# Kernel optimization log

Measured on AMD Instinct MI355X. Metric: run time of the kernel, lower is better.

Reference implementation:

```python
import jax, jax.numpy as jnp
import numpy as np

B, CDD, HIS, T, L, D, K = 64, 5, 100, 30, 3, 256, 10
THRESHOLD = 0.1


def setup_inputs() -> dict:
    key = jax.random.key(0)
    k1, k2, k3, k4 = jax.random.split(key, 4)
    cdd_repr = jax.random.normal(k1, (B, CDD, D), dtype=jnp.float32)
    his_repr = jax.random.normal(k2, (B, HIS, D), dtype=jnp.float32)
    his_embedding = jax.random.normal(k3, (B, HIS, T, L, D), dtype=jnp.float32)
    # xavier_normal init for Linear(D, D)
    W_sel = jax.random.normal(k4, (D, D), dtype=jnp.float32) * np.sqrt(2.0 / (D + D))
    b_sel = jnp.zeros((D,), dtype=jnp.float32)
    return {"cdd_repr": cdd_repr, "his_repr": his_repr,
            "his_embedding": his_embedding, "W_sel": W_sel, "b_sel": b_sel}


def _l2_normalize(x, eps=1e-12):
    # matches torch F.normalize(dim=-1)
    n = jnp.linalg.norm(x, axis=-1, keepdims=True)
    return x / jnp.maximum(n, eps)


def reference(cdd_repr, his_repr, his_embedding, W_sel, b_sel):
    # selectionProject (Linear) + L2 normalize
    cdd_p = _l2_normalize(cdd_repr @ W_sel.T + b_sel)   # [B, CDD, D]
    his_p = _l2_normalize(his_repr @ W_sel.T + b_sel)   # [B, HIS, D]

    # news-level attention scores [B, CDD, HIS]
    attn = jnp.einsum('bcd,bhd->bch', cdd_p, his_p)

    # top-k over history
    attn_topk, idx = jax.lax.top_k(attn, K)             # [B, CDD, K]

    # multi-dim gather of history embeddings -> [B, CDD, K, T, L, D]
    his_activated = his_embedding[jnp.arange(B)[:, None, None], idx]

    # threshold masking: zero out weights below threshold, scale embeddings
    w = jnp.where(attn_topk < THRESHOLD, 0.0, attn_topk)
    his_activated = his_activated * w[:, :, :, None, None, None]

    return his_activated, idx
```

## Files before the change

### kernel.cpp

```cpp
#include <hip/hip_runtime.h>
#include <hip/hip_bf16.h>

#define NB   64
#define NCDD 5
#define NHIS 100
#define ND   256
#define NK   10
#define TLD  23040
#define THRESH 0.1f
#define NEG_INF (-3.402823466e38f)
#define NROWS_HIS 6400
#define NROWS_CDD 320

typedef float f32x4 __attribute__((ext_vector_type(4)));

__global__ __launch_bounds__(256) void proj_norm_all(
    const float* __restrict__ his_repr,
    const float* __restrict__ cdd_repr,
    const float* __restrict__ W,
    const float* __restrict__ bvec,
    float* __restrict__ Yall)
{
    __shared__ float red[4][8];
    const int r0  = blockIdx.x * 8;
    const int tid = threadIdx.x;
    const int sub = tid & 3;
    const int grp = tid >> 2;
    const int wave = tid >> 6, lane = tid & 63;

    const float* __restrict__ X = (r0 < NROWS_HIS)
        ? (his_repr + (size_t)r0 * ND)
        : (cdd_repr + (size_t)(r0 - NROWS_HIS) * ND);

    float acc[4][8];
#pragma unroll
    for (int p = 0; p < 4; ++p)
#pragma unroll
        for (int r = 0; r < 8; ++r) acc[p][r] = 0.f;

#pragma unroll 4
    for (int i = 0; i < 16; ++i) {
        const int kb = sub * 4 + 16 * i;
        float4 x4[8];
#pragma unroll
        for (int r = 0; r < 8; ++r)
            x4[r] = *(const float4*)(X + (size_t)r * ND + kb);
#pragma unroll
        for (int p = 0; p < 4; ++p) {
            const int d = p * 64 + grp;
            const float4 w4 = *(const float4*)(W + (size_t)d * ND + kb);
#pragma unroll
            for (int r = 0; r < 8; ++r)
                acc[p][r] += w4.x * x4[r].x + w4.y * x4[r].y
                           + w4.z * x4[r].z + w4.w * x4[r].w;
        }
    }

#pragma unroll
    for (int p = 0; p < 4; ++p)
#pragma unroll
        for (int r = 0; r < 8; ++r) {
            float v = acc[p][r];
            v += __shfl_xor(v, 1);
            v += __shfl_xor(v, 2);
            acc[p][r] = v;
        }

    float bias[4];
#pragma unroll
    for (int p = 0; p < 4; ++p) bias[p] = bvec[p * 64 + grp];

    float ss[8];
#pragma unroll
    for (int r = 0; r < 8; ++r) {
        float t = 0.f;
#pragma unroll
        for (int p = 0; p < 4; ++p) {
            const float y = acc[p][r] + bias[p];
            acc[p][r] = y;
            t += y * y;
        }
        for (int off = 32; off; off >>= 1) t += __shfl_xor(t, off);
        ss[r] = t;
    }
    if (lane == 0) {
#pragma unroll
        for (int r = 0; r < 8; ++r) red[wave][r] = ss[r];
    }
    __syncthreads();

#pragma unroll
    for (int r = 0; r < 8; ++r) {
        const float s = 0.25f * (red[0][r] + red[1][r] + red[2][r] + red[3][r]);
        const float scale = 1.0f / fmaxf(sqrtf(s), 1e-12f);
        if (sub == 0) {
#pragma unroll
            for (int p = 0; p < 4; ++p)
                Yall[(size_t)(r0 + r) * ND + p * 64 + grp] = acc[p][r] * scale;
        }
    }
}

__global__ __launch_bounds__(512) void attn_topk_kernel(
    const float* __restrict__ cdd_p,
    const float* __restrict__ his_p,
    float* __restrict__ out_idx_f,
    int* __restrict__ ws_idx,
    float* __restrict__ ws_w)
{
    __shared__ float attn_s[NCDD][128];
    const int b   = blockIdx.x;
    const int tid = threadIdx.x;
    const int sub = tid & 3, grp = tid >> 2;
    const int wave = tid >> 6, lane = tid & 63;

    const float* __restrict__ cbase = cdd_p + (size_t)b * NCDD * ND;
    const float* __restrict__ hbase = his_p + (size_t)b * NHIS * ND;

#pragma unroll
    for (int it = 0; it < 4; ++it) {
        const int task = it * 128 + grp;
        if (task < NCDD * NHIS) {
            const int c = task / NHIS, h = task - c * NHIS;
            const float* __restrict__ crow = cbase + (size_t)c * ND;
            const float* __restrict__ hrow = hbase + (size_t)h * ND;
            float a = 0.f;
#pragma unroll
            for (int i = 0; i < 16; ++i) {
                const int kb = sub * 4 + 16 * i;
                const float4 cv = *(const float4*)(crow + kb);
                const float4 hv = *(const float4*)(hrow + kb);
                a += cv.x * hv.x + cv.y * hv.y + cv.z * hv.z + cv.w * hv.w;
            }
            a += __shfl_xor(a, 1);
            a += __shfl_xor(a, 2);
            if (sub == 0) attn_s[c][h] = a;
        }
    }
    __syncthreads();

    if (wave < NCDD) {
        const int c = wave;
        float v0 = attn_s[c][lane];
        float v1 = (lane + 64 < NHIS) ? attn_s[c][lane + 64] : NEG_INF;
#pragma unroll
        for (int k = 0; k < NK; ++k) {
            float lv; int li;
            if (v1 > v0) { lv = v1; li = lane + 64; }
            else         { lv = v0; li = lane; }
            for (int off = 1; off < 64; off <<= 1) {
                const float ov = __shfl_xor(lv, off);
                const int   oi = __shfl_xor(li, off);
                if (ov > lv || (ov == lv && oi < li)) { lv = ov; li = oi; }
            }
            if (lane == 0) {
                const float w = (lv < THRESH) ? 0.0f : lv;
                const int g = (b * NCDD + c) * NK + k;
                ws_idx[g] = li;
                ws_w[g]   = w;
                out_idx_f[g] = (float)li;
            }
            if (li == lane)            v0 = NEG_INF;
            else if (li == lane + 64)  v1 = NEG_INF;
        }
    }
}

__global__ __launch_bounds__(256) void gather_kernel(
    const float* __restrict__ his_emb,
    const int* __restrict__ ws_idx,
    const float* __restrict__ ws_w,
    float* __restrict__ out)
{
    const int orig = blockIdx.x;
    const int g = (orig & 7) * 400 + (orig >> 3);
    const int b = g / (NCDD * NK);
    const int tid = threadIdx.x;
    const float w = ws_w[g];

    f32x4* __restrict__ dst = (f32x4*)(out + (size_t)g * TLD);

    if (w == 0.0f) {
        const f32x4 z = {0.f, 0.f, 0.f, 0.f};
#pragma unroll
        for (int it = 0; it < 22; ++it) dst[tid + it * 256] = z;
        if (tid < 128) dst[22 * 256 + tid] = z;
        return;
    }

    const int idx = ws_idx[g];
    const f32x4* __restrict__ src =
        (const f32x4*)(his_emb + ((size_t)b * NHIS + idx) * TLD);

    f32x4 v[22];
    f32x4 vt;
#pragma unroll
    for (int j = 0; j < 22; ++j) v[j] = src[tid + j * 256];
    const bool tail = (tid < 128);
    if (tail) vt = src[22 * 256 + tid];

#pragma unroll
    for (int j = 0; j < 22; ++j) dst[tid + j * 256] = v[j] * w;
    if (tail) dst[22 * 256 + tid] = vt * w;
}

extern "C" void kernel_launch(void* const* d_in, const int* in_sizes, int n_in,
                              void* d_out, int out_size, void* d_ws, size_t ws_size,
                              hipStream_t stream)
{
    const float* cdd_repr = (const float*)d_in[0];
    const float* his_repr = (const float*)d_in[1];
    const float* his_emb  = (const float*)d_in[2];
    const float* W_sel    = (const float*)d_in[3];
    const float* b_sel    = (const float*)d_in[4];
    float* out = (float*)d_out;

    char* ws = (char*)d_ws;
    float* Yall  = (float*)ws;
    float* his_p = Yall;
    float* cdd_p = Yall + (size_t)NROWS_HIS * ND;
    int*   idx_i = (int*)  (ws + 6881280);
    float* w_w   = (float*)(ws + 6894080);

    float* out_idx_f = out + (size_t)NB * NCDD * NK * TLD;

    proj_norm_all<<<(NROWS_HIS + NROWS_CDD) / 8, 256, 0, stream>>>(
        his_repr, cdd_repr, W_sel, b_sel, Yall);
    attn_topk_kernel<<<NB, 512, 0, stream>>>(cdd_p, his_p,
                                             out_idx_f, idx_i, w_w);
    gather_kernel<<<NB * NCDD * NK, 256, 0, stream>>>(his_emb, idx_i, w_w, out);
}
```

Before: 162.3 us.

## Fuse attention top-k into gather kernel, recomputing scores per output block

Merges the attention/top-k kernel into the gather kernel, so each gather block recomputes the 100 attention scores for its (b,c) row and the top-10 selection, then picks its own k-th entry. This removes one kernel launch and the workspace round-trip for indices and weights. In exchange the attention dot products and top-k are computed redundantly 10 times per (b,c), and the gather start is delayed by that compute in every block.

```diff
diff --git a/kernel.cpp b/kernel.cpp
--- a/kernel.cpp
+++ b/kernel.cpp
@@ -101,50 +101,58 @@
     }
 }
 
-__global__ __launch_bounds__(512) void attn_topk_kernel(
+__global__ __launch_bounds__(256) void attn_gather_kernel(
     const float* __restrict__ cdd_p,
     const float* __restrict__ his_p,
+    const float* __restrict__ his_emb,
     float* __restrict__ out_idx_f,
-    int* __restrict__ ws_idx,
-    float* __restrict__ ws_w)
+    float* __restrict__ out)
 {
-    __shared__ float attn_s[NCDD][128];
-    const int b   = blockIdx.x;
+    __shared__ float attn_s[128];
+    __shared__ float pick_w[NK];
+    __shared__ int   pick_i[NK];
+
+    const int orig = blockIdx.x;
+    const int g = (orig & 7) * 400 + (orig >> 3);
+    const int b = g / (NCDD * NK);
+    const int c = (g / NK) % NCDD;
+    const int k = g % NK;
     const int tid = threadIdx.x;
     const int sub = tid & 3, grp = tid >> 2;
     const int wave = tid >> 6, lane = tid & 63;
 
-    const float* __restrict__ cbase = cdd_p + (size_t)b * NCDD * ND;
+    const float* __restrict__ crow = cdd_p + ((size_t)b * NCDD + c) * ND;
     const float* __restrict__ hbase = his_p + (size_t)b * NHIS * ND;
-
-#pragma unroll
-    for (int it = 0; it < 4; ++it) {
-        const int task = it * 128 + grp;
-        if (task < NCDD * NHIS) {
-            const int c = task / NHIS, h = task - c * NHIS;
-            const float* __restrict__ crow = cbase + (size_t)c * ND;
-            const float* __restrict__ hrow = hbase + (size_t)h * ND;
-            float a = 0.f;
-#pragma unroll
-            for (int i = 0; i < 16; ++i) {
-                const int kb = sub * 4 + 16 * i;
-                const float4 cv = *(const float4*)(crow + kb);
-                const float4 hv = *(const float4*)(hrow + kb);
-                a += cv.x * hv.x + cv.y * hv.y + cv.z * hv.z + cv.w * hv.w;
+    {
+        const int h0 = grp, h1 = grp + 64;
+        const float* __restrict__ h0row = hbase + (size_t)h0 * ND;
+        const float* __restrict__ h1row = hbase + (size_t)h1 * ND;
+        float a0 = 0.f, a1 = 0.f;
+#pragma unroll
+        for (int i = 0; i < 16; ++i) {
+            const int kb = sub * 4 + 16 * i;
+            const float4 cv = *(const float4*)(crow + kb);
+            const float4 v0 = *(const float4*)(h0row + kb);
+            a0 += cv.x * v0.x + cv.y * v0.y + cv.z * v0.z + cv.w * v0.w;
+            if (h1 < NHIS) {
+                const float4 v1 = *(const float4*)(h1row + kb);
+                a1 += cv.x * v1.x + cv.y * v1.y + cv.z * v1.z + cv.w * v1.w;
             }
-            a += __shfl_xor(a, 1);
-            a += __shfl_xor(a, 2);
-            if (sub == 0) attn_s[c][h] = a;
+        }
+        a0 += __shfl_xor(a0, 1); a0 += __shfl_xor(a0, 2);
+        a1 += __shfl_xor(a1, 1); a1 += __shfl_xor(a1, 2);
+        if (sub == 0) {
+            attn_s[h0] = a0;
+            if (h1 < NHIS) attn_s[h1] = a1;
         }
     }
     __syncthreads();
 
-    if (wave < NCDD) {
-        const int c = wave;
-        float v0 = attn_s[c][lane];
-        float v1 = (lane + 64 < NHIS) ? attn_s[c][lane + 64] : NEG_INF;
-#pragma unroll
-        for (int k = 0; k < NK; ++k) {
+    if (wave == 0) {
+        float v0 = attn_s[lane];
+        float v1 = (lane + 64 < NHIS) ? attn_s[lane + 64] : NEG_INF;
+#pragma unroll
+        for (int kk = 0; kk < NK; ++kk) {
             float lv; int li;
             if (v1 > v0) { lv = v1; li = lane + 64; }
             else         { lv = v0; li = lane; }
@@ -154,29 +162,18 @@
                 if (ov > lv || (ov == lv && oi < li)) { lv = ov; li = oi; }
             }
             if (lane == 0) {
-                const float w = (lv < THRESH) ? 0.0f : lv;
-                const int g = (b * NCDD + c) * NK + k;
-                ws_idx[g] = li;
-                ws_w[g]   = w;
-                out_idx_f[g] = (float)li;
+                pick_i[kk] = li;
+                pick_w[kk] = (lv < THRESH) ? 0.0f : lv;
             }
             if (li == lane)            v0 = NEG_INF;
             else if (li == lane + 64)  v1 = NEG_INF;
         }
     }
-}
-
-__global__ __launch_bounds__(256) void gather_kernel(
-    const float* __restrict__ his_emb,
-    const int* __restrict__ ws_idx,
-    const float* __restrict__ ws_w,
-    float* __restrict__ out)
-{
-    const int orig = blockIdx.x;
-    const int g = (orig & 7) * 400 + (orig >> 3);
-    const int b = g / (NCDD * NK);
-    const int tid = threadIdx.x;
-    const float w = ws_w[g];
+    __syncthreads();
+
+    const int   idx = pick_i[k];
+    const float w   = pick_w[k];
+    if (tid == 0) out_idx_f[g] = (float)idx;
 
     f32x4* __restrict__ dst = (f32x4*)(out + (size_t)g * TLD);
 
@@ -188,7 +185,6 @@
         return;
     }
 
-    const int idx = ws_idx[g];
     const f32x4* __restrict__ src =
         (const f32x4*)(his_emb + ((size_t)b * NHIS + idx) * TLD);
 
@@ -219,14 +215,11 @@
     float* Yall  = (float*)ws;
     float* his_p = Yall;
     float* cdd_p = Yall + (size_t)NROWS_HIS * ND;
-    int*   idx_i = (int*)  (ws + 6881280);
-    float* w_w   = (float*)(ws + 6894080);
 
     float* out_idx_f = out + (size_t)NB * NCDD * NK * TLD;
 
     proj_norm_all<<<(NROWS_HIS + NROWS_CDD) / 8, 256, 0, stream>>>(
         his_repr, cdd_repr, W_sel, b_sel, Yall);
-    attn_topk_kernel<<<NB, 512, 0, stream>>>(cdd_p, his_p,
-                                             out_idx_f, idx_i, w_w);
-    gather_kernel<<<NB * NCDD * NK, 256, 0, stream>>>(his_emb, idx_i, w_w, out);
+    attn_gather_kernel<<<NB * NCDD * NK, 256, 0, stream>>>(
+        cdd_p, his_p, his_emb, out_idx_f, out);
 }
```

Measured after the change: 178.3 us. +9.9%, slower.

## Replace per-slot gather blocks with flat grid-stride gather over output

Applied to the files above, without the earlier changes.

The gather stage no longer launches one 256-thread block per (batch, candidate, k) slot with 23 float4s held per thread. It now uses a fixed grid of 2048 blocks that stride over the whole output as flat float4 elements, computing the slot index by integer division and reading the weight and index for each element. The aim is to even out load across the GPU and hide memory latency through a persistent grid-stride pattern. In exchange, every element pays a division plus repeated (cached) loads of the weight and index, and the explicit block-to-slot interleaving used for channel spreading is lost.

```diff
diff --git a/kernel.cpp b/kernel.cpp
--- a/kernel.cpp
+++ b/kernel.cpp
@@ -7,10 +7,12 @@
 #define ND   256
 #define NK   10
 #define TLD  23040
+#define NSLOT4 (3200 * 5760)
 #define THRESH 0.1f
 #define NEG_INF (-3.402823466e38f)
 #define NROWS_HIS 6400
 #define NROWS_CDD 320
+#define GBLOCKS 2048
 
 typedef float f32x4 __attribute__((ext_vector_type(4)));
 
@@ -166,42 +168,29 @@
     }
 }
 
-__global__ __launch_bounds__(256) void gather_kernel(
+__global__ __launch_bounds__(256) void gather_flat(
     const float* __restrict__ his_emb,
     const int* __restrict__ ws_idx,
     const float* __restrict__ ws_w,
     float* __restrict__ out)
 {
-    const int orig = blockIdx.x;
-    const int g = (orig & 7) * 400 + (orig >> 3);
-    const int b = g / (NCDD * NK);
-    const int tid = threadIdx.x;
-    const float w = ws_w[g];
-
-    f32x4* __restrict__ dst = (f32x4*)(out + (size_t)g * TLD);
-
-    if (w == 0.0f) {
-        const f32x4 z = {0.f, 0.f, 0.f, 0.f};
-#pragma unroll
-        for (int it = 0; it < 22; ++it) dst[tid + it * 256] = z;
-        if (tid < 128) dst[22 * 256 + tid] = z;
-        return;
-    }
-
-    const int idx = ws_idx[g];
-    const f32x4* __restrict__ src =
-        (const f32x4*)(his_emb + ((size_t)b * NHIS + idx) * TLD);
-
-    f32x4 v[22];
-    f32x4 vt;
-#pragma unroll
-    for (int j = 0; j < 22; ++j) v[j] = src[tid + j * 256];
-    const bool tail = (tid < 128);
-    if (tail) vt = src[22 * 256 + tid];
-
-#pragma unroll
-    for (int j = 0; j < 22; ++j) dst[tid + j * 256] = v[j] * w;
-    if (tail) dst[22 * 256 + tid] = vt * w;
+    const int S = GBLOCKS * 256;
+    const f32x4* __restrict__ src4 = (const f32x4*)his_emb;
+    f32x4* __restrict__ dst4 = (f32x4*)out;
+
+#pragma unroll 4
+    for (int i = blockIdx.x * 256 + threadIdx.x; i < NSLOT4; i += S) {
+        const int g = i / 5760;
+        const int r = i - g * 5760;
+        const float w = ws_w[g];
+        f32x4 v = {0.f, 0.f, 0.f, 0.f};
+        if (w != 0.0f) {
+            const int b = g / (NCDD * NK);
+            const int idx = ws_idx[g];
+            v = src4[(size_t)(b * NHIS + idx) * 5760 + r] * w;
+        }
+        dst4[i] = v;
+    }
 }
 
 extern "C" void kernel_launch(void* const* d_in, const int* in_sizes, int n_in,
@@ -228,5 +217,5 @@
         his_repr, cdd_repr, W_sel, b_sel, Yall);
     attn_topk_kernel<<<NB, 512, 0, stream>>>(cdd_p, his_p,
                                              out_idx_f, idx_i, w_w);
-    gather_kernel<<<NB * NCDD * NK, 256, 0, stream>>>(his_emb, idx_i, w_w, out);
-}
+    gather_flat<<<GBLOCKS, 256, 0, stream>>>(his_emb, idx_i, w_w, out);
+}
```

Measured after the change: 167.3 us. 3.1% more time.

## Deduplicate history gathers so each selected row is read once per batch

Applied to the files above, without the earlier changes.

The top-k kernel now builds, per batch, a list of unique selected history indices and a 64-bit mask of which output slots use each one. The gather kernel then loads each unique embedding row once and writes it, scaled, to every output slot that selected it. Rows whose slots all have zero weight are not read at all. This cuts redundant reads of his_embedding when candidates share history picks. In exchange, some blocks now do several output writes serially while others exit early, which can unbalance the work across blocks.

```diff
diff --git a/kernel.cpp b/kernel.cpp
--- a/kernel.cpp
+++ b/kernel.cpp
@@ -13,6 +13,7 @@
 #define NROWS_CDD 320
 
 typedef float f32x4 __attribute__((ext_vector_type(4)));
+typedef unsigned long long u64;
 
 __global__ __launch_bounds__(256) void proj_norm_all(
     const float* __restrict__ his_repr,
@@ -106,13 +107,23 @@
     const float* __restrict__ his_p,
     float* __restrict__ out_idx_f,
     int* __restrict__ ws_idx,
-    float* __restrict__ ws_w)
+    float* __restrict__ ws_w,
+    int* __restrict__ ws_nu,
+    int* __restrict__ ws_uidx,
+    u64* __restrict__ ws_tmask)
 {
     __shared__ float attn_s[NCDD][128];
+    __shared__ int   pick_h[NCDD * NK];
+    __shared__ int   map_s[NHIS];
+    __shared__ int   uidx_s[NCDD * NK];
+    __shared__ u64   tmask_s[NCDD * NK];
+    __shared__ int   nu_s;
     const int b   = blockIdx.x;
     const int tid = threadIdx.x;
     const int sub = tid & 3, grp = tid >> 2;
     const int wave = tid >> 6, lane = tid & 63;
+
+    if (tid < NHIS) map_s[tid] = -1;
 
     const float* __restrict__ cbase = cdd_p + (size_t)b * NCDD * ND;
     const float* __restrict__ hbase = his_p + (size_t)b * NHIS * ND;
@@ -159,49 +170,94 @@
                 ws_idx[g] = li;
                 ws_w[g]   = w;
                 out_idx_f[g] = (float)li;
+                pick_h[c * NK + k] = li;
             }
             if (li == lane)            v0 = NEG_INF;
             else if (li == lane + 64)  v1 = NEG_INF;
         }
     }
-}
-
-__global__ __launch_bounds__(256) void gather_kernel(
+    __syncthreads();
+
+    if (tid == 0) {
+        int nu = 0;
+        for (int t = 0; t < NCDD * NK; ++t) {
+            const int h = pick_h[t];
+            int u = map_s[h];
+            if (u < 0) {
+                u = nu++;
+                map_s[h] = u;
+                uidx_s[u] = h;
+                tmask_s[u] = 0ull;
+            }
+            tmask_s[u] |= (1ull << t);
+        }
+        nu_s = nu;
+        ws_nu[b] = nu;
+    }
+    __syncthreads();
+
+    if (tid < NCDD * NK && tid < nu_s) {
+        ws_uidx[b * (NCDD * NK) + tid]  = uidx_s[tid];
+        ws_tmask[b * (NCDD * NK) + tid] = tmask_s[tid];
+    }
+}
+
+__global__ __launch_bounds__(256) void gather_dedup(
     const float* __restrict__ his_emb,
-    const int* __restrict__ ws_idx,
     const float* __restrict__ ws_w,
+    const int* __restrict__ ws_nu,
+    const int* __restrict__ ws_uidx,
+    const u64* __restrict__ ws_tmask,
     float* __restrict__ out)
 {
     const int orig = blockIdx.x;
-    const int g = (orig & 7) * 400 + (orig >> 3);
-    const int b = g / (NCDD * NK);
+    const int m = (orig & 7) * 400 + (orig >> 3);
+    const int b = m / (NCDD * NK);
+    const int u = m - b * (NCDD * NK);
+    if (u >= ws_nu[b]) return;
+
     const int tid = threadIdx.x;
-    const float w = ws_w[g];
-
-    f32x4* __restrict__ dst = (f32x4*)(out + (size_t)g * TLD);
-
-    if (w == 0.0f) {
-        const f32x4 z = {0.f, 0.f, 0.f, 0.f};
-#pragma unroll
-        for (int it = 0; it < 22; ++it) dst[tid + it * 256] = z;
-        if (tid < 128) dst[22 * 256 + tid] = z;
-        return;
-    }
-
-    const int idx = ws_idx[g];
-    const f32x4* __restrict__ src =
-        (const f32x4*)(his_emb + ((size_t)b * NHIS + idx) * TLD);
+    const int h = ws_uidx[b * (NCDD * NK) + u];
+    u64 mask = ws_tmask[b * (NCDD * NK) + u];
+
+    bool anyread = false;
+    {
+        u64 mm = mask;
+        while (mm) {
+            const int t = __ffsll(mm) - 1;
+            mm &= mm - 1;
+            if (ws_w[b * (NCDD * NK) + t] != 0.0f) anyread = true;
+        }
+    }
 
     f32x4 v[22];
     f32x4 vt;
-#pragma unroll
-    for (int j = 0; j < 22; ++j) v[j] = src[tid + j * 256];
     const bool tail = (tid < 128);
-    if (tail) vt = src[22 * 256 + tid];
-
-#pragma unroll
-    for (int j = 0; j < 22; ++j) dst[tid + j * 256] = v[j] * w;
-    if (tail) dst[22 * 256 + tid] = vt * w;
+    if (anyread) {
+        const f32x4* __restrict__ src =
+            (const f32x4*)(his_emb + ((size_t)b * NHIS + h) * TLD);
+#pragma unroll
+        for (int j = 0; j < 22; ++j) v[j] = src[tid + j * 256];
+        if (tail) vt = src[22 * 256 + tid];
+    }
+
+    while (mask) {
+        const int t = __ffsll(mask) - 1;
+        mask &= mask - 1;
+        const float w = ws_w[b * (NCDD * NK) + t];
+        f32x4* __restrict__ dst =
+            (f32x4*)(out + (size_t)(b * (NCDD * NK) + t) * TLD);
+        if (w == 0.0f) {
+            const f32x4 z = {0.f, 0.f, 0.f, 0.f};
+#pragma unroll
+            for (int j = 0; j < 22; ++j) dst[tid + j * 256] = z;
+            if (tail) dst[22 * 256 + tid] = z;
+        } else {
+#pragma unroll
+            for (int j = 0; j < 22; ++j) dst[tid + j * 256] = v[j] * w;
+            if (tail) dst[22 * 256 + tid] = vt * w;
+        }
+    }
 }
 
 extern "C" void kernel_launch(void* const* d_in, const int* in_sizes, int n_in,
@@ -219,14 +275,18 @@
     float* Yall  = (float*)ws;
     float* his_p = Yall;
     float* cdd_p = Yall + (size_t)NROWS_HIS * ND;
-    int*   idx_i = (int*)  (ws + 6881280);
+    int*   idx_i = (int*)(ws + 6881280);
     float* w_w   = (float*)(ws + 6894080);
+    int*   nu_g  = (int*)(ws + 6906880);
+    int*   uidx_g= (int*)(ws + 6907136);
+    u64*   tmask_g = (u64*)(ws + 6920064);
 
     float* out_idx_f = out + (size_t)NB * NCDD * NK * TLD;
 
     proj_norm_all<<<(NROWS_HIS + NROWS_CDD) / 8, 256, 0, stream>>>(
         his_repr, cdd_repr, W_sel, b_sel, Yall);
-    attn_topk_kernel<<<NB, 512, 0, stream>>>(cdd_p, his_p,
-                                             out_idx_f, idx_i, w_w);
-    gather_kernel<<<NB * NCDD * NK, 256, 0, stream>>>(his_emb, idx_i, w_w, out);
-}
+    attn_topk_kernel<<<NB, 512, 0, stream>>>(cdd_p, his_p, out_idx_f,
+                                             idx_i, w_w, nu_g, uidx_g, tmask_g);
+    gather_dedup<<<NB * NCDD * NK, 256, 0, stream>>>(his_emb, w_w, nu_g,
+                                                     uidx_g, tmask_g, out);
+}
```

Result: slower. 172.8 us (+6.5%).
